# Performance work log

Hardware: AMD Instinct MI355X
Metric: run time of the kernel (lower is better)

Reference implementation:

```python
import jax, jax.numpy as jnp
import numpy as np

D_MODEL = 2048
NUM_HEADS = 16
FAN = 4
HEAD = D_MODEL // NUM_HEADS
EPS = 1e-5


def _layernorm(x):
    # LayerNorm over last dim, no affine params (elementwise_affine=False)
    mu = jnp.mean(x, axis=-1, keepdims=True)
    var = jnp.mean(jnp.square(x - mu), axis=-1, keepdims=True)
    return (x - mu) * jax.lax.rsqrt(var + EPS)


def setup_inputs() -> dict:
    key = jax.random.key(0)
    k0, k1, k2, k3, k4 = jax.random.split(key, 5)
    B, T = 2, 2048
    qkv_out = 3 * D_MODEL + FAN * D_MODEL  # 14336
    s_in = 1.0 / np.sqrt(D_MODEL)
    s_h = 1.0 / np.sqrt(FAN * D_MODEL)
    return {
        "inputs": jax.random.normal(k0, (B, T, D_MODEL), dtype=jnp.float32),
        "W_qkv": jax.random.normal(k1, (D_MODEL, qkv_out), dtype=jnp.float32) * s_in,
        "b_qkv": jax.random.normal(k2, (qkv_out,), dtype=jnp.float32) * 0.01,
        "W_mlp": jax.random.normal(k3, (FAN * D_MODEL, D_MODEL), dtype=jnp.float32) * s_h,
        "b_mlp": jax.random.normal(k4, (D_MODEL,), dtype=jnp.float32) * 0.01,
    }


def reference(inputs, W_qkv, b_qkv, W_mlp, b_mlp):
    B, T, C = inputs.shape
    # parallel QKV + MLP hidden projection on pre-LN input
    x = _layernorm(inputs)
    qkv_hidden = jnp.einsum("btc,cf->btf", x, W_qkv) + b_qkv
    q = qkv_hidden[..., :D_MODEL]
    k = qkv_hidden[..., D_MODEL:2 * D_MODEL]
    v = qkv_hidden[..., 2 * D_MODEL:3 * D_MODEL]
    hidden = qkv_hidden[..., 3 * D_MODEL:]

    # split heads: (B, H, T, head)
    def to_heads(t):
        return t.reshape(B, T, NUM_HEADS, HEAD).transpose(0, 2, 1, 3)

    q = _layernorm(to_heads(q))  # QK-LayerNorm over head dim
    k = _layernorm(to_heads(k))
    v = to_heads(v)

    # MLP branch (exact GELU, torch default)
    mlp_out = jnp.einsum("bth,hc->btc", jax.nn.gelu(hidden, approximate=False), W_mlp) + b_mlp

    # causal attention
    logits = jnp.einsum("bhqd,bhkd->bhqk", q, k) * (HEAD ** -0.5)
    causal = jnp.tril(jnp.ones((T, T), dtype=bool))
    logits = jnp.where(causal, logits, -jnp.inf)
    scores = jax.nn.softmax(logits, axis=-1)
    outs = jnp.einsum("bhqk,bhkd->bhqd", scores, v)
    outs = outs.transpose(0, 2, 1, 3).reshape(B, T, C)

    return outs + mlp_out + inputs
```

## Files before the change

### kernel.cpp

```cpp
#include <hip/hip_runtime.h>
#include <hip/hip_bf16.h>
#include <math.h>

typedef __bf16 bf16;
typedef __bf16 bf16x4 __attribute__((ext_vector_type(4)));
typedef __bf16 bf16x8 __attribute__((ext_vector_type(8)));
typedef unsigned short u16x8 __attribute__((ext_vector_type(8)));
typedef float f32x4 __attribute__((ext_vector_type(4)));

#define MFMA16(a, b, c) __builtin_amdgcn_mfma_f32_16x16x32_bf16((a), (b), (c), 0, 0, 0)

__device__ __forceinline__ void llds16(const void* g, void* l) {
  __builtin_amdgcn_global_load_lds(
      (const __attribute__((address_space(1))) unsigned*)g,
      (__attribute__((address_space(3))) unsigned*)l, 16, 0, 0);
}

__global__ __launch_bounds__(256) void transpose_cvt(const float* __restrict__ src,
                                                     bf16* __restrict__ dst, int R, int C) {
  __shared__ float tile[32][33];
  const int bx = blockIdx.x * 32, by = blockIdx.y * 32;
  const int tx = threadIdx.x, ty = threadIdx.y;
#pragma unroll
  for (int i = 0; i < 32; i += 8)
    tile[ty + i][tx] = src[(size_t)(by + ty + i) * C + bx + tx];
  __syncthreads();
#pragma unroll
  for (int i = 0; i < 32; i += 8)
    dst[(size_t)(bx + ty + i) * R + by + tx] = (bf16)tile[tx][ty + i];
}

__global__ __launch_bounds__(256) void ln_rows(const float* __restrict__ x,
                                               bf16* __restrict__ y) {
  const int r = blockIdx.x, t = threadIdx.x;
  const float* xr = x + (size_t)r * 2048;
  f32x4 a = ((const f32x4*)xr)[t];
  f32x4 b = ((const f32x4*)xr)[t + 256];
  float s = 0.f, ss = 0.f;
#pragma unroll
  for (int j = 0; j < 4; ++j) {
    s += a[j] + b[j];
    ss += a[j] * a[j] + b[j] * b[j];
  }
#pragma unroll
  for (int m = 1; m < 64; m <<= 1) {
    s += __shfl_xor(s, m, 64);
    ss += __shfl_xor(ss, m, 64);
  }
  __shared__ float red[8];
  const int wv = t >> 6;
  if ((t & 63) == 0) { red[wv] = s; red[4 + wv] = ss; }
  __syncthreads();
  s = red[0] + red[1] + red[2] + red[3];
  ss = red[4] + red[5] + red[6] + red[7];
  const float mu = s * (1.f / 2048.f);
  const float var = ss * (1.f / 2048.f) - mu * mu;
  const float rs = rsqrtf(var + 1e-5f);
  bf16x4 o1, o2;
#pragma unroll
  for (int j = 0; j < 4; ++j) {
    o1[j] = (bf16)((a[j] - mu) * rs);
    o2[j] = (bf16)((b[j] - mu) * rs);
  }
  bf16* yr = y + (size_t)r * 2048;
  ((bf16x4*)yr)[t] = o1;
  ((bf16x4*)yr)[t + 256] = o2;
}

template <int MODE, int BN>
__global__ __launch_bounds__(512, 2) void gemm8p(
    const bf16* __restrict__ A, const bf16* __restrict__ B, void* __restrict__ Cp,
    const int K, const int lda, const int ldb, const int ldc,
    const float* __restrict__ bias, const float* __restrict__ res1,
    const float* __restrict__ res2, const int gx) {
  constexpr int WN = BN / 4;
  constexpr int NR = WN / 16;
  constexpr int NRH = NR / 2;
  constexpr int NLB = BN / 128;
  constexpr int BUFSZ = 8192 + NLB * 4096;
  __shared__ bf16 lds[4 * BUFSZ];

  const int t = threadIdx.x, w = t >> 6, l = t & 63;
  const int l16 = l & 15, lg = l >> 4;
  const int wm = w >> 2, wn = w & 3;
  const int nwg = gridDim.x;
  const int id = (blockIdx.x & 7) * (nwg >> 3) + (blockIdx.x >> 3);
  const int by = id / gx, bx = id - by * gx;
  const int m0 = by * 256, n0 = bx * BN;
  const int NT = K >> 5;

  auto stage = [&](int kt) {
    bf16* Ab = lds + (size_t)(kt & 3) * BUFSZ;
    bf16* Bb = Ab + 8192;
    const int k0 = kt << 5;
    const int r4 = t >> 2;
    const int cg = (t & 3) ^ ((t >> 3) & 3);
#pragma unroll
    for (int j = 0; j < 2; ++j)
      llds16(A + (size_t)(m0 + j * 128 + r4) * lda + k0 + cg * 8, Ab + j * 4096 + t * 8);
#pragma unroll
    for (int j = 0; j < NLB; ++j)
      llds16(B + (size_t)(n0 + j * 128 + r4) * ldb + k0 + cg * 8, Bb + j * 4096 + t * 8);
  };

  f32x4 acc[8][NR] = {};
  stage(0); stage(1); stage(2);
  if constexpr (BN == 256) asm volatile("s_waitcnt vmcnt(8)" ::: "memory");
  else                     asm volatile("s_waitcnt vmcnt(6)" ::: "memory");
  __builtin_amdgcn_s_barrier();

  const int arow = wm * 128 + l16;
  const int brow = wn * WN + l16;
  const int slot = (lg ^ ((l16 >> 1) & 3)) * 8;

  for (int kt = 0; kt < NT; ++kt) {
    const bf16* Ab = lds + (size_t)(kt & 3) * BUFSZ;
    const bf16* Bb = Ab + 8192;
    if (kt + 3 < NT) stage(kt + 3);
    bf16x8 af[8], bfr[NR];
#pragma unroll
    for (int mi = 0; mi < 8; ++mi)
      af[mi] = *(const bf16x8*)(Ab + (arow + mi * 16) * 32 + slot);
#pragma unroll
    for (int ni = 0; ni < NRH; ++ni)
      bfr[ni] = *(const bf16x8*)(Bb + (brow + ni * 16) * 32 + slot);
    __builtin_amdgcn_s_setprio(1);
#pragma unroll
    for (int mi = 0; mi < 8; ++mi)
#pragma unroll
      for (int ni = 0; ni < NRH; ++ni)
        acc[mi][ni] = MFMA16(af[mi], bfr[ni], acc[mi][ni]);
    __builtin_amdgcn_s_setprio(0);
#pragma unroll
    for (int ni = NRH; ni < NR; ++ni)
      bfr[ni] = *(const bf16x8*)(Bb + (brow + ni * 16) * 32 + slot);
    __builtin_amdgcn_s_setprio(1);
#pragma unroll
    for (int mi = 0; mi < 8; ++mi)
#pragma unroll
      for (int ni = NRH; ni < NR; ++ni)
        acc[mi][ni] = MFMA16(af[mi], bfr[ni], acc[mi][ni]);
    __builtin_amdgcn_s_setprio(0);
    if (kt < NT - 1) {
      const int staged = (kt + 3 < NT) ? kt + 3 : NT - 1;
      const int infl = staged - (kt + 1);
      if (infl >= 2) {
        if constexpr (BN == 256) asm volatile("s_waitcnt vmcnt(8)" ::: "memory");
        else                     asm volatile("s_waitcnt vmcnt(6)" ::: "memory");
      } else if (infl == 1) {
        if constexpr (BN == 256) asm volatile("s_waitcnt vmcnt(4)" ::: "memory");
        else                     asm volatile("s_waitcnt vmcnt(3)" ::: "memory");
      } else {
        asm volatile("s_waitcnt vmcnt(0)" ::: "memory");
      }
      __builtin_amdgcn_s_barrier();
    }
  }

  const int crow0 = m0 + wm * 128 + lg * 4;
  const int ccol0 = n0 + wn * WN + l16;
  if constexpr (MODE == 0) {
    bf16* C = (bf16*)Cp;
#pragma unroll
    for (int ni = 0; ni < NR; ++ni) {
      const float bv = bias[ccol0 + ni * 16];
#pragma unroll
      for (int mi = 0; mi < 8; ++mi)
#pragma unroll
        for (int r = 0; r < 4; ++r)
          C[(size_t)(crow0 + mi * 16 + r) * ldc + ccol0 + ni * 16] =
              (bf16)(acc[mi][ni][r] + bv);
    }
  } else {
    float* C = (float*)Cp;
#pragma unroll
    for (int ni = 0; ni < NR; ++ni) {
      const float bv = bias[ccol0 + ni * 16];
#pragma unroll
      for (int mi = 0; mi < 8; ++mi)
#pragma unroll
        for (int r = 0; r < 4; ++r) {
          const size_t idx = (size_t)(crow0 + mi * 16 + r) * ldc + ccol0 + ni * 16;
          C[idx] = acc[mi][ni][r] + bv + res1[idx] + res2[idx];
        }
    }
  }
}

__global__ __launch_bounds__(256) void post1(bf16* __restrict__ qkv) {
  const int r = blockIdx.x, t = threadIdx.x, w = t >> 6, l = t & 63;
  bf16* row = qkv + (size_t)r * 14336;
#pragma unroll
  for (int gi = 0; gi < 8; ++gi) {
    const int g = w + gi * 4;
    bf16* p = row + g * 128 + l * 2;
    const float a = (float)p[0], b = (float)p[1];
    float s = a + b, ss = a * a + b * b;
#pragma unroll
    for (int m = 1; m < 64; m <<= 1) {
      s += __shfl_xor(s, m, 64);
      ss += __shfl_xor(ss, m, 64);
    }
    const float mu = s * (1.f / 128.f);
    const float var = ss * (1.f / 128.f) - mu * mu;
    const float rs = rsqrtf(var + 1e-5f);
    p[0] = (bf16)((a - mu) * rs);
    p[1] = (bf16)((b - mu) * rs);
  }
  bf16* hb = row + 6144;
#pragma unroll
  for (int i = 0; i < 8; ++i) {
    const int idx = t + i * 256;
    bf16x4 v = ((bf16x4*)hb)[idx];
#pragma unroll
    for (int j = 0; j < 4; ++j) {
      float f = (float)v[j];
      f = 0.5f * f * (1.f + erff(f * 0.70710678118f));
      v[j] = (bf16)f;
    }
    ((bf16x4*)hb)[idx] = v;
  }
}

__global__ __launch_bounds__(256) void attn_kernel(const bf16* __restrict__ qkv,
                                                   float* __restrict__ attn_out) {
  __shared__ bf16 K_lds[32][136];
  __shared__ bf16 V_lds[128][40];
  __shared__ bf16 P_lds[4][16][40];
  const int t = threadIdx.x, w = t >> 6, l = t & 63;
  const int l16 = l & 15, lg = l >> 4;
  const int b = blockIdx.y >> 4, h = blockIdx.y & 15;
  const int qb0 = blockIdx.x * 64;
  const int tq0 = qb0 + w * 16;
  const size_t bT = (size_t)b * 2048;
  const int LDQ = 14336;
  const size_t qoff = (size_t)h * 128;
  const size_t koff = 2048 + (size_t)h * 128;
  const size_t voff = 4096 + (size_t)h * 128;
  const float SCALE = 0.08838834764831845f;

  bf16x8 qf[4];
  {
    const bf16* qrow = qkv + (bT + tq0 + l16) * LDQ + qoff + lg * 8;
#pragma unroll
    for (int dc = 0; dc < 4; ++dc) qf[dc] = *(const bf16x8*)(qrow + dc * 32);
  }
  float m_r[4], l_r[4];
  f32x4 accO[8] = {};
#pragma unroll
  for (int r = 0; r < 4; ++r) { m_r[r] = -1e30f; l_r[r] = 0.f; }

  const int nkv = (qb0 >> 5) + 2;
  for (int kt = 0; kt < nkv; ++kt) {
    const int kt0 = kt << 5;
    __syncthreads();
#pragma unroll
    for (int it = 0; it < 2; ++it) {
      const int c = it * 256 + t;
      const int krow = c >> 4, c8 = (c & 15) * 8;
      *(bf16x8*)(&K_lds[krow][c8]) =
          *(const bf16x8*)(qkv + (bT + kt0 + krow) * LDQ + koff + c8);
    }
    {
      const int kp = (t & 15) * 2, dg = (t >> 4) * 8;
      const bf16* g0 = qkv + (bT + kt0 + kp) * LDQ + voff + dg;
      u16x8 v0 = *(const u16x8*)g0;
      u16x8 v1 = *(const u16x8*)(g0 + LDQ);
#pragma unroll
      for (int j = 0; j < 8; ++j) {
        const unsigned pk = (unsigned)v0[j] | ((unsigned)v1[j] << 16);
        *(unsigned*)(&V_lds[dg + j][kp]) = pk;
      }
    }
    __syncthreads();
    if (kt0 <= tq0 + 15) {
      f32x4 sacc[2] = {};
#pragma unroll
      for (int dc = 0; dc < 4; ++dc) {
        bf16x8 kf = *(const bf16x8*)(&K_lds[l16][dc * 32 + lg * 8]);
        sacc[0] = MFMA16(qf[dc], kf, sacc[0]);
      }
#pragma unroll
      for (int dc = 0; dc < 4; ++dc) {
        bf16x8 kf = *(const bf16x8*)(&K_lds[16 + l16][dc * 32 + lg * 8]);
        sacc[1] = MFMA16(qf[dc], kf, sacc[1]);
      }
      float s0[4], s1[4];
      const bool need_mask = (kt0 + 31 > tq0);
#pragma unroll
      for (int r = 0; r < 4; ++r) {
        s0[r] = sacc[0][r] * SCALE;
        s1[r] = sacc[1][r] * SCALE;
      }
      if (need_mask) {
#pragma unroll
        for (int r = 0; r < 4; ++r) {
          const int q = tq0 + lg * 4 + r;
          if (kt0 + l16 > q) s0[r] = -1e30f;
          if (kt0 + 16 + l16 > q) s1[r] = -1e30f;
        }
      }
      float pmax[4];
#pragma unroll
      for (int r = 0; r < 4; ++r) pmax[r] = fmaxf(s0[r], s1[r]);
#pragma unroll
      for (int m = 1; m < 16; m <<= 1)
#pragma unroll
        for (int r = 0; r < 4; ++r) pmax[r] = fmaxf(pmax[r], __shfl_xor(pmax[r], m, 64));
      float fr[4];
#pragma unroll
      for (int r = 0; r < 4; ++r) {
        const float mn = fmaxf(m_r[r], pmax[r]);
        fr[r] = __expf(m_r[r] - mn);
        m_r[r] = mn;
      }
      float p0[4], p1[4], rsum[4];
#pragma unroll
      for (int r = 0; r < 4; ++r) {
        p0[r] = __expf(s0[r] - m_r[r]);
        p1[r] = __expf(s1[r] - m_r[r]);
        rsum[r] = p0[r] + p1[r];
      }
#pragma unroll
      for (int m = 1; m < 16; m <<= 1)
#pragma unroll
        for (int r = 0; r < 4; ++r) rsum[r] += __shfl_xor(rsum[r], m, 64);
#pragma unroll
      for (int r = 0; r < 4; ++r) l_r[r] = l_r[r] * fr[r] + rsum[r];
#pragma unroll
      for (int f = 0; f < 8; ++f)
#pragma unroll
        for (int r = 0; r < 4; ++r) accO[f][r] *= fr[r];
#pragma unroll
      for (int r = 0; r < 4; ++r) {
        P_lds[w][lg * 4 + r][l16] = (bf16)p0[r];
        P_lds[w][lg * 4 + r][16 + l16] = (bf16)p1[r];
      }
      bf16x8 pa = *(const bf16x8*)(&P_lds[w][l16][lg * 8]);
#pragma unroll
      for (int f = 0; f < 8; ++f) {
        bf16x8 vf = *(const bf16x8*)(&V_lds[f * 16 + l16][lg * 8]);
        accO[f] = MFMA16(pa, vf, accO[f]);
      }
    }
  }
  float inv[4];
#pragma unroll
  for (int r = 0; r < 4; ++r) inv[r] = 1.0f / l_r[r];
  float* orow = attn_out + (bT + tq0 + lg * 4) * 2048 + (size_t)h * 128 + l16;
#pragma unroll
  for (int f = 0; f < 8; ++f)
#pragma unroll
    for (int r = 0; r < 4; ++r) orow[(size_t)r * 2048 + f * 16] = accO[f][r] * inv[r];
}

extern "C" void kernel_launch(void* const* d_in, const int* in_sizes, int n_in,
                              void* d_out, int out_size, void* d_ws, size_t ws_size,
                              hipStream_t stream) {
  const float* inputs = (const float*)d_in[0];
  const float* W_qkv = (const float*)d_in[1];
  const float* b_qkv = (const float*)d_in[2];
  const float* W_mlp = (const float*)d_in[3];
  const float* b_mlp = (const float*)d_in[4];
  float* out = (float*)d_out;

  char* ws = (char*)d_ws;
  bf16* Wqkv_t = (bf16*)ws;
  bf16* Wmlp_t = (bf16*)(ws + 58720256);
  bf16* x_ln = (bf16*)(ws + 92274688);
  bf16* qkv = (bf16*)(ws + 109051904);
  float* attn = (float*)(ws + 226492416);

  transpose_cvt<<<dim3(14336 / 32, 2048 / 32), dim3(32, 8), 0, stream>>>(W_qkv, Wqkv_t,
                                                                         2048, 14336);
  transpose_cvt<<<dim3(2048 / 32, 8192 / 32), dim3(32, 8), 0, stream>>>(W_mlp, Wmlp_t,
                                                                        8192, 2048);
  ln_rows<<<4096, 256, 0, stream>>>(inputs, x_ln);
  gemm8p<0, 256><<<896, 512, 0, stream>>>(x_ln, Wqkv_t, qkv, 2048, 2048, 2048, 14336,
                                          b_qkv, nullptr, nullptr, 56);
  post1<<<4096, 256, 0, stream>>>(qkv);
  attn_kernel<<<dim3(32, 32), 256, 0, stream>>>(qkv, attn);
  gemm8p<1, 128><<<256, 512, 0, stream>>>(qkv + 6144, Wmlp_t, out, 8192, 14336, 8192,
                                          2048, b_mlp, inputs, attn, 16);
}
```

Baseline: 960.4 us.

## Split GEMM tile staging into A/B halves interleaved with MFMA phases

Measured after the change: 961.1 us. About the same (+0.1%).

```diff
diff --git a/kernel.cpp b/kernel.cpp
--- a/kernel.cpp
+++ b/kernel.cpp
@@ -75,8 +75,8 @@
     const float* __restrict__ res2, const int gx) {
   constexpr int WN = BN / 4;
   constexpr int NR = WN / 16;
-  constexpr int NRH = NR / 2;
   constexpr int NLB = BN / 128;
+  constexpr int LPT = 2 + NLB;
   constexpr int BUFSZ = 8192 + NLB * 4096;
   __shared__ bf16 lds[4 * BUFSZ];
 
@@ -89,24 +89,27 @@
   const int m0 = by * 256, n0 = bx * BN;
   const int NT = K >> 5;
 
-  auto stage = [&](int kt) {
+  const int r4 = t >> 2;
+  const int cg = (t & 3) ^ ((t >> 3) & 3);
+
+  auto stageA = [&](int kt) {
     bf16* Ab = lds + (size_t)(kt & 3) * BUFSZ;
-    bf16* Bb = Ab + 8192;
     const int k0 = kt << 5;
-    const int r4 = t >> 2;
-    const int cg = (t & 3) ^ ((t >> 3) & 3);
 #pragma unroll
     for (int j = 0; j < 2; ++j)
       llds16(A + (size_t)(m0 + j * 128 + r4) * lda + k0 + cg * 8, Ab + j * 4096 + t * 8);
+  };
+  auto stageB = [&](int kt) {
+    bf16* Bb = lds + (size_t)(kt & 3) * BUFSZ + 8192;
+    const int k0 = kt << 5;
 #pragma unroll
     for (int j = 0; j < NLB; ++j)
       llds16(B + (size_t)(n0 + j * 128 + r4) * ldb + k0 + cg * 8, Bb + j * 4096 + t * 8);
   };
 
   f32x4 acc[8][NR] = {};
-  stage(0); stage(1); stage(2);
-  if constexpr (BN == 256) asm volatile("s_waitcnt vmcnt(8)" ::: "memory");
-  else                     asm volatile("s_waitcnt vmcnt(6)" ::: "memory");
+  stageA(0); stageB(0); stageA(1); stageB(1); stageA(2); stageB(2);
+  asm volatile("s_waitcnt vmcnt(%0)" ::"n"(2 * LPT) : "memory");
   __builtin_amdgcn_s_barrier();
 
   const int arow = wm * 128 + l16;
@@ -116,45 +119,44 @@
   for (int kt = 0; kt < NT; ++kt) {
     const bf16* Ab = lds + (size_t)(kt & 3) * BUFSZ;
     const bf16* Bb = Ab + 8192;
-    if (kt + 3 < NT) stage(kt + 3);
-    bf16x8 af[8], bfr[NR];
-#pragma unroll
-    for (int mi = 0; mi < 8; ++mi)
+    const bool pre = (kt + 3 < NT);
+    bf16x8 af[4], ah[4], bfr[NR];
+#pragma unroll
+    for (int mi = 0; mi < 4; ++mi)
       af[mi] = *(const bf16x8*)(Ab + (arow + mi * 16) * 32 + slot);
 #pragma unroll
-    for (int ni = 0; ni < NRH; ++ni)
+    for (int ni = 0; ni < NR; ++ni)
       bfr[ni] = *(const bf16x8*)(Bb + (brow + ni * 16) * 32 + slot);
+    if (pre) stageA(kt + 3);
+    __builtin_amdgcn_s_barrier();
     __builtin_amdgcn_s_setprio(1);
 #pragma unroll
-    for (int mi = 0; mi < 8; ++mi)
-#pragma unroll
-      for (int ni = 0; ni < NRH; ++ni)
+    for (int mi = 0; mi < 4; ++mi)
+#pragma unroll
+      for (int ni = 0; ni < NR; ++ni)
         acc[mi][ni] = MFMA16(af[mi], bfr[ni], acc[mi][ni]);
     __builtin_amdgcn_s_setprio(0);
-#pragma unroll
-    for (int ni = NRH; ni < NR; ++ni)
-      bfr[ni] = *(const bf16x8*)(Bb + (brow + ni * 16) * 32 + slot);
+    __builtin_amdgcn_s_barrier();
+#pragma unroll
+    for (int mi = 0; mi < 4; ++mi)
+      ah[mi] = *(const bf16x8*)(Ab + (arow + (mi + 4) * 16) * 32 + slot);
+    if (pre) stageB(kt + 3);
+    __builtin_amdgcn_s_barrier();
     __builtin_amdgcn_s_setprio(1);
 #pragma unroll
-    for (int mi = 0; mi < 8; ++mi)
-#pragma unroll
-      for (int ni = NRH; ni < NR; ++ni)
-        acc[mi][ni] = MFMA16(af[mi], bfr[ni], acc[mi][ni]);
+    for (int mi = 0; mi < 4; ++mi)
+#pragma unroll
+      for (int ni = 0; ni < NR; ++ni)
+        acc[mi + 4][ni] = MFMA16(ah[mi], bfr[ni], acc[mi + 4][ni]);
     __builtin_amdgcn_s_setprio(0);
     if (kt < NT - 1) {
-      const int staged = (kt + 3 < NT) ? kt + 3 : NT - 1;
+      const int staged = pre ? kt + 3 : NT - 1;
       const int infl = staged - (kt + 1);
-      if (infl >= 2) {
-        if constexpr (BN == 256) asm volatile("s_waitcnt vmcnt(8)" ::: "memory");
-        else                     asm volatile("s_waitcnt vmcnt(6)" ::: "memory");
-      } else if (infl == 1) {
-        if constexpr (BN == 256) asm volatile("s_waitcnt vmcnt(4)" ::: "memory");
-        else                     asm volatile("s_waitcnt vmcnt(3)" ::: "memory");
-      } else {
-        asm volatile("s_waitcnt vmcnt(0)" ::: "memory");
-      }
-      __builtin_amdgcn_s_barrier();
-    }
+      if (infl >= 2)      asm volatile("s_waitcnt vmcnt(%0)" ::"n"(2 * LPT) : "memory");
+      else if (infl == 1) asm volatile("s_waitcnt vmcnt(%0)" ::"n"(LPT) : "memory");
+      else                asm volatile("s_waitcnt vmcnt(0)" ::: "memory");
+    }
+    __builtin_amdgcn_s_barrier();
   }
 
   const int crow0 = m0 + wm * 128 + lg * 4;
```
